# Kernel tuning notes

Measured on AMD Instinct MI355X. Metric: run time of the kernel, lower is better.

Reference implementation:

```python
import jax, jax.numpy as jnp
import numpy as np
import math

DIM = 768
HIDDEN = 3072
HEADS = 8
DEPTH = DIM // HEADS
EPS = 1e-5


def gelu_tanh(x):
    c = math.sqrt(2.0 / math.pi)
    return x * 0.5 * (1.0 + jnp.tanh(c * (x + 0.044715 * jnp.power(x, 3))))


def layer_norm(x, g, b):
    mu = jnp.mean(x, axis=-1, keepdims=True)
    var = jnp.mean(jnp.square(x - mu), axis=-1, keepdims=True)
    return (x - mu) * jax.lax.rsqrt(var + EPS) * g + b


def setup_inputs() -> dict:
    key = jax.random.key(0)
    ks = jax.random.split(key, 12)
    B, F, N = 2, 64, 128
    s = 0.02
    return {
        "q": jax.random.normal(ks[0], (B, F, N, DIM), jnp.float32),
        "k": jax.random.normal(ks[1], (B, F, N, DIM), jnp.float32),
        "v": jax.random.normal(ks[2], (B, F, N, DIM), jnp.float32),
        "ln1_g": jnp.ones((DIM,), jnp.float32),
        "ln1_b": jnp.zeros((DIM,), jnp.float32),
        "wq": jax.random.normal(ks[3], (DIM, DIM), jnp.float32) * s,
        "wk": jax.random.normal(ks[4], (DIM, DIM), jnp.float32) * s,
        "wv": jax.random.normal(ks[5], (DIM, DIM), jnp.float32) * s,
        "wo": jax.random.normal(ks[6], (DIM, DIM), jnp.float32) * s,
        "wo_b": jnp.zeros((DIM,), jnp.float32),
        "ln2_g": jnp.ones((DIM,), jnp.float32),
        "ln2_b": jnp.zeros((DIM,), jnp.float32),
        "w1": jax.random.normal(ks[7], (DIM, HIDDEN), jnp.float32) * s,
        "b1": jnp.zeros((HIDDEN,), jnp.float32),
        "w2": jax.random.normal(ks[8], (HIDDEN, DIM), jnp.float32) * s,
        "b2": jnpp if False else jnp.zeros((DIM,), jnp.float32),
    }


def reference(q, k, v, ln1_g, ln1_b, wq, wk, wv, wo, wo_b, ln2_g, ln2_b, w1, b1, w2, b2):
    # Shared norm1 applied to q, k, v (same params, as in the original)
    qn = layer_norm(q, ln1_g, ln1_b)
    kn = layer_norm(k, ln1_g, ln1_b)
    vn = layer_norm(v, ln1_g, ln1_b)

    B, F, N, _ = qn.shape
    # Projections (no bias on wq/wk/wv since att_bias=False)
    def split_heads(x):
        return x.reshape(B, F, N, HEADS, DEPTH).transpose(0, 1, 3, 2, 4)  # b f h n d

    qh = split_heads(qn @ wq)
    kh = split_heads(kn @ wk)
    vh = split_heads(vn @ wv)

    scale = DEPTH ** (-0.5)
    dots = jnp.einsum('bfhid,bfhjd->bfhij', qh, kh) * scale
    att_weight = jax.nn.softmax(dots, axis=-1)
    out = jnp.einsum('bfhij,bfhjd->bfhid', att_weight, vh)
    out = out.transpose(0, 1, 3, 2, 4).reshape(B, F, N, DIM)
    y = out @ wo + wo_b

    y = y + qn  # residual with normed q
    h = gelu_tanh(layer_norm(y, ln2_g, ln2_b) @ w1 + b1)
    out2 = h @ w2 + b2
    return out2 + y, att_weight
```

## Files before the change

kernel.cpp:

```cpp
#include <hip/hip_runtime.h>


#define NROWS 16384
#define TDIM 768
#define THID 3072
#define EPS 1e-5f

typedef short bf16x8 __attribute__((ext_vector_type(8)));
typedef float f32x4 __attribute__((ext_vector_type(4)));

__device__ __forceinline__ float b2f(unsigned short u) {
    union { unsigned int i; float f; } v; v.i = ((unsigned int)u) << 16; return v.f;
}
__device__ __forceinline__ unsigned short f2b(float f) {
    union { float f; unsigned int i; } v; v.f = f;
    unsigned int r = v.i + 0x7fffu + ((v.i >> 16) & 1u);
    return (unsigned short)(r >> 16);
}

__device__ __forceinline__ void async_copy16(const unsigned short* g, unsigned short* l) {
    __builtin_amdgcn_global_load_lds(
        (const __attribute__((address_space(1))) unsigned int*)g,
        (__attribute__((address_space(3))) unsigned int*)l,
        16, 0, 0);
}

__global__ __launch_bounds__(256) void cvt_t_kernel(
    const float* __restrict__ src, unsigned short* __restrict__ dst, int K, int N)
{
    __shared__ unsigned short tile[32][33];
    int n0 = blockIdx.x * 32, k0 = blockIdx.y * 32;
    int tx = threadIdx.x & 31, ty = threadIdx.x >> 5;
#pragma unroll
    for (int r = ty; r < 32; r += 8)
        tile[r][tx] = f2b(src[(size_t)(k0 + r) * N + n0 + tx]);
    __syncthreads();
#pragma unroll
    for (int r = ty; r < 32; r += 8)
        dst[(size_t)(n0 + r) * K + k0 + tx] = tile[tx][r];
}

template<bool IN_F32>
__global__ __launch_bounds__(256) void ln_kernel(
    const void* __restrict__ x0, const void* __restrict__ x1,
    const void* __restrict__ x2,
    const float* __restrict__ g, const float* __restrict__ bb,
    unsigned short* __restrict__ o0, unsigned short* __restrict__ o1,
    unsigned short* __restrict__ o2)
{
    int t = blockIdx.y;
    const void* x = (t == 0) ? x0 : (t == 1) ? x1 : x2;
    unsigned short* o = (t == 0) ? o0 : (t == 1) ? o1 : o2;
    size_t base = (size_t)blockIdx.x * TDIM;
    int tid = threadIdx.x;
    float v[3]; float sum = 0.f, sq = 0.f;
#pragma unroll
    for (int i = 0; i < 3; i++) {
        if constexpr (IN_F32) v[i] = ((const float*)x)[base + tid + i * 256];
        else v[i] = b2f(((const unsigned short*)x)[base + tid + i * 256]);
        sum += v[i]; sq += v[i] * v[i];
    }
#pragma unroll
    for (int o_ = 32; o_ > 0; o_ >>= 1) {
        sum += __shfl_down(sum, o_); sq += __shfl_down(sq, o_);
    }
    __shared__ float s1[4], s2[4];
    __shared__ float smu, srs;
    int wave = tid >> 6, lane = tid & 63;
    if (lane == 0) { s1[wave] = sum; s2[wave] = sq; }
    __syncthreads();
    if (tid == 0) {
        float S = s1[0] + s1[1] + s1[2] + s1[3];
        float Q = s2[0] + s2[1] + s2[2] + s2[3];
        float mu = S / (float)TDIM;
        float var = Q / (float)TDIM - mu * mu;
        smu = mu; srs = rsqrtf(var + EPS);
    }
    __syncthreads();
    float mu = smu, rs = srs;
#pragma unroll
    for (int i = 0; i < 3; i++) {
        int c = tid + i * 256;
        o[base + c] = f2b((v[i] - mu) * rs * g[c] + bb[c]);
    }
}

template<bool BIAS, bool RES, bool GELU, bool OUTF32>
__global__ __launch_bounds__(256) void gemm_kernel(
    const unsigned short* __restrict__ A, const unsigned short* __restrict__ BT,
    const float* __restrict__ bias, const unsigned short* __restrict__ resid,
    void* __restrict__ Cv, int M, int N, int K,
    size_t aStride, size_t bStride, size_t cStride)
{
    __shared__ unsigned short sA[128][32];
    __shared__ unsigned short sB[128][32];
    int tid = threadIdx.x;

    int nbx = gridDim.x;
    int nwg = nbx * gridDim.y;
    int bid = blockIdx.y * nbx + blockIdx.x;
    int xcd = bid & 7, loc = bid >> 3;
    int qc = nwg >> 3, rc = nwg & 7;
    int swz = (xcd < rc ? xcd * (qc + 1) : rc * (qc + 1) + (xcd - rc) * qc) + loc;
    int row0 = (swz / nbx) * 128;
    int col0 = (swz % nbx) * 128;

    int z = blockIdx.z;
    A  += (size_t)z * aStride;
    BT += (size_t)z * bStride;
    size_t zoff = (size_t)z * cStride;

    int wave = tid >> 6, lane = tid & 63;
    int wm = (wave >> 1) * 64, wn = (wave & 1) * 64;
    int cl = lane & 15, quad = lane >> 4;

    f32x4 acc[4][4];
#pragma unroll
    for (int i = 0; i < 4; i++)
#pragma unroll
        for (int j = 0; j < 4; j++) acc[i][j] = (f32x4){0.f, 0.f, 0.f, 0.f};

    const unsigned short* Arow = A + (size_t)row0 * K;
    const unsigned short* Brow = BT + (size_t)col0 * K;

    int c0 = wave * 128 + lane, c1 = c0 + 64;
    const unsigned short* aS0 = Arow + (size_t)(c0 >> 2) * K + ((c0 & 3) << 3);
    const unsigned short* aS1 = Arow + (size_t)(c1 >> 2) * K + ((c1 & 3) << 3);
    const unsigned short* bS0 = Brow + (size_t)(c0 >> 2) * K + ((c0 & 3) << 3);
    const unsigned short* bS1 = Brow + (size_t)(c1 >> 2) * K + ((c1 & 3) << 3);
    unsigned short* aD0 = &sA[0][0] + (size_t)(wave * 128) * 8;
    unsigned short* aD1 = aD0 + 64 * 8;
    unsigned short* bD0 = &sB[0][0] + (size_t)(wave * 128) * 8;
    unsigned short* bD1 = bD0 + 64 * 8;

    for (int k0 = 0; k0 < K; k0 += 32) {
        async_copy16(aS0 + k0, aD0);
        async_copy16(aS1 + k0, aD1);
        async_copy16(bS0 + k0, bD0);
        async_copy16(bS1 + k0, bD1);
        __syncthreads();
        bf16x8 af[4], bfr[4];
#pragma unroll
        for (int mi = 0; mi < 4; mi++)
            af[mi] = *(const bf16x8*)(&sA[wm + mi * 16 + cl][quad * 8]);
#pragma unroll
        for (int ni = 0; ni < 4; ni++)
            bfr[ni] = *(const bf16x8*)(&sB[wn + ni * 16 + cl][quad * 8]);
#pragma unroll
        for (int mi = 0; mi < 4; mi++)
#pragma unroll
            for (int ni = 0; ni < 4; ni++)
                acc[mi][ni] = __builtin_amdgcn_mfma_f32_16x16x32_bf16(
                    af[mi], bfr[ni], acc[mi][ni], 0, 0, 0);
        __syncthreads();
    }

    float bvv[4];
#pragma unroll
    for (int ni = 0; ni < 4; ni++) {
        if constexpr (BIAS) bvv[ni] = bias[col0 + wn + ni * 16 + cl];
        else bvv[ni] = 0.f;
    }
#pragma unroll
    for (int mi = 0; mi < 4; mi++) {
#pragma unroll
        for (int r = 0; r < 4; r++) {
            int gr = row0 + wm + mi * 16 + quad * 4 + r;
            size_t rb = (size_t)gr * N + col0 + wn + cl;
#pragma unroll
            for (int ni = 0; ni < 4; ni++) {
                float v = acc[mi][ni][r];
                if constexpr (BIAS) v += bvv[ni];
                if constexpr (GELU) {
                    float x = v;
                    float t = x + 0.044715f * x * x * x;
                    float e = __expf(-1.5957691216057308f * t);
                    v = x * __builtin_amdgcn_rcpf(1.0f + e);
                }
                if constexpr (RES) v += b2f(resid[rb + ni * 16]);
                size_t idx = rb + ni * 16 + zoff;
                if constexpr (OUTF32) ((float*)Cv)[idx] = v;
                else ((unsigned short*)Cv)[idx] = f2b(v);
            }
        }
    }
}

template<bool BIAS, bool GELU>
__global__ __launch_bounds__(512) void gemm256_kernel(
    const unsigned short* __restrict__ A, const unsigned short* __restrict__ BT,
    const float* __restrict__ bias, unsigned short* __restrict__ C,
    int N, int K)
{
    __shared__ unsigned short sA[2][256][32];
    __shared__ unsigned short sB[2][256][32];
    int tid = threadIdx.x;

    int nbx = gridDim.x;
    int nwg = nbx * gridDim.y;
    int bid = blockIdx.y * nbx + blockIdx.x;
    int xcd = bid & 7, loc = bid >> 3;
    int qc = nwg >> 3, rc = nwg & 7;
    int swz = (xcd < rc ? xcd * (qc + 1) : rc * (qc + 1) + (xcd - rc) * qc) + loc;
    int row0 = (swz / nbx) * 256;
    int col0 = (swz % nbx) * 256;

    int wave = tid >> 6, lane = tid & 63;
    int wr = wave >> 2, wc = wave & 3;
    int cl = lane & 15, quad = lane >> 4;
    int sl8 = (quad ^ ((cl >> 1) & 3)) << 3;

    size_t rowoff = (size_t)(tid >> 2) * K + (size_t)(((tid & 3) ^ ((tid >> 3) & 3)) << 3);
    const unsigned short* aS0 = A + (size_t)row0 * K + rowoff;
    const unsigned short* aS1 = aS0 + (size_t)128 * K;
    const unsigned short* bS0 = BT + (size_t)col0 * K + rowoff;
    const unsigned short* bS1 = bS0 + (size_t)128 * K;
    unsigned short* aD = &sA[0][0][0] + (wave * 64) * 8;
    unsigned short* bD = &sB[0][0][0] + (wave * 64) * 8;

    f32x4 acc[8][4];
#pragma unroll
    for (int i = 0; i < 8; i++)
#pragma unroll
        for (int j = 0; j < 4; j++) acc[i][j] = (f32x4){0.f, 0.f, 0.f, 0.f};

    int NT = K >> 5;
    async_copy16(aS0, aD);
    async_copy16(aS1, aD + 4096);
    async_copy16(bS0, bD);
    async_copy16(bS1, bD + 4096);

    for (int t = 0; t < NT; ++t) {
        int cur = t & 1;
        if (t + 1 < NT) {
            int nb = (cur ^ 1) * 8192;
            int ko = (t + 1) << 5;
            async_copy16(aS0 + ko, aD + nb);
            async_copy16(aS1 + ko, aD + nb + 4096);
            async_copy16(bS0 + ko, bD + nb);
            async_copy16(bS1 + ko, bD + nb + 4096);
            asm volatile("s_waitcnt vmcnt(4)" ::: "memory");
        } else {
            asm volatile("s_waitcnt vmcnt(0)" ::: "memory");
        }
        __builtin_amdgcn_s_barrier();
        __builtin_amdgcn_sched_barrier(0);
        const unsigned short* pA = &sA[cur][0][0];
        const unsigned short* pB = &sB[cur][0][0];
        bf16x8 bfr[4], af[4];
#pragma unroll
        for (int ni = 0; ni < 4; ni++)
            bfr[ni] = *(const bf16x8*)(pB + (wc * 64 + ni * 16 + cl) * 32 + sl8);
#pragma unroll
        for (int mi = 0; mi < 4; mi++)
            af[mi] = *(const bf16x8*)(pA + (wr * 128 + mi * 16 + cl) * 32 + sl8);
#pragma unroll
        for (int mi = 0; mi < 4; mi++)
#pragma unroll
            for (int ni = 0; ni < 4; ni++)
                acc[mi][ni] = __builtin_amdgcn_mfma_f32_16x16x32_bf16(
                    af[mi], bfr[ni], acc[mi][ni], 0, 0, 0);
#pragma unroll
        for (int mi = 0; mi < 4; mi++)
            af[mi] = *(const bf16x8*)(pA + (wr * 128 + 64 + mi * 16 + cl) * 32 + sl8);
#pragma unroll
        for (int mi = 0; mi < 4; mi++)
#pragma unroll
            for (int ni = 0; ni < 4; ni++)
                acc[mi + 4][ni] = __builtin_amdgcn_mfma_f32_16x16x32_bf16(
                    af[mi], bfr[ni], acc[mi + 4][ni], 0, 0, 0);
        __builtin_amdgcn_sched_barrier(0);
        __builtin_amdgcn_s_barrier();
        __builtin_amdgcn_sched_barrier(0);
    }

    float bvv[4];
#pragma unroll
    for (int ni = 0; ni < 4; ni++) {
        if constexpr (BIAS) bvv[ni] = bias[col0 + wc * 64 + ni * 16 + cl];
        else bvv[ni] = 0.f;
    }
#pragma unroll
    for (int mi = 0; mi < 8; mi++) {
#pragma unroll
        for (int r = 0; r < 4; r++) {
            int gr = row0 + wr * 128 + mi * 16 + quad * 4 + r;
            size_t rb = (size_t)gr * N + col0 + wc * 64 + cl;
#pragma unroll
            for (int ni = 0; ni < 4; ni++) {
                float v = acc[mi][ni][r] + bvv[ni];
                if constexpr (GELU) {
                    float x = v;
                    float tt = x + 0.044715f * x * x * x;
                    float e = __expf(-1.5957691216057308f * tt);
                    v = x * __builtin_amdgcn_rcpf(1.0f + e);
                }
                C[rb + ni * 16] = f2b(v);
            }
        }
    }
}

__global__ __launch_bounds__(256) void attn_fused_kernel(
    const unsigned short* __restrict__ qh, const unsigned short* __restrict__ kh,
    const unsigned short* __restrict__ vh, float* __restrict__ att,
    unsigned short* __restrict__ attout)
{
    __shared__ __align__(16) unsigned short smem[30464];
    __shared__ float wmax[2][128];
    __shared__ float wsum[2][128];
    __shared__ float sInv[128];
    unsigned short* sQ = smem;
    unsigned short* sK = smem + 12288;
    unsigned short* sP = smem;
    unsigned short* sVt = smem + 17408;

    int hb = blockIdx.x, g = hb >> 3, h = hb & 7;
    int tid = threadIdx.x;
    int wave = tid >> 6, lane = tid & 63;
    int cl = lane & 15, quad = lane >> 4;
    int wm = (wave >> 1) * 64, wn = (wave & 1) * 64;

    size_t rbase = (size_t)g * 128 * TDIM + (size_t)h * 96;

#pragma unroll
    for (int it = 0; it < 6; it++) {
        int cb = wave * 384 + it * 64;
        int c = cb + lane;
        int r = c / 12, dc = (c % 12) * 8;
        async_copy16(qh + rbase + (size_t)r * TDIM + dc, sQ + (size_t)cb * 8);
        async_copy16(kh + rbase + (size_t)r * TDIM + dc, sK + (size_t)cb * 8);
    }
    __syncthreads();

    f32x4 acc[4][4];
#pragma unroll
    for (int i = 0; i < 4; i++)
#pragma unroll
        for (int j = 0; j < 4; j++) acc[i][j] = (f32x4){0.f, 0.f, 0.f, 0.f};
#pragma unroll
    for (int kk = 0; kk < 3; kk++) {
        bf16x8 af[4], bfr[4];
#pragma unroll
        for (int mi = 0; mi < 4; mi++)
            af[mi] = *(const bf16x8*)(sQ + (size_t)(wm + mi * 16 + cl) * 96 + kk * 32 + quad * 8);
#pragma unroll
        for (int ni = 0; ni < 4; ni++)
            bfr[ni] = *(const bf16x8*)(sK + (size_t)(wn + ni * 16 + cl) * 96 + kk * 32 + quad * 8);
#pragma unroll
        for (int mi = 0; mi < 4; mi++)
#pragma unroll
            for (int ni = 0; ni < 4; ni++)
                acc[mi][ni] = __builtin_amdgcn_mfma_f32_16x16x32_bf16(
                    af[mi], bfr[ni], acc[mi][ni], 0, 0, 0);
    }

    const float scale = 0.10206207261596575f;
#pragma unroll
    for (int mi = 0; mi < 4; mi++)
#pragma unroll
        for (int ni = 0; ni < 4; ni++)
#pragma unroll
            for (int r = 0; r < 4; r++) acc[mi][ni][r] *= scale;
#pragma unroll
    for (int mi = 0; mi < 4; mi++) {
#pragma unroll
        for (int r = 0; r < 4; r++) {
            float m = fmaxf(fmaxf(acc[mi][0][r], acc[mi][1][r]),
                            fmaxf(acc[mi][2][r], acc[mi][3][r]));
            m = fmaxf(m, __shfl_xor(m, 1));
            m = fmaxf(m, __shfl_xor(m, 2));
            m = fmaxf(m, __shfl_xor(m, 4));
            m = fmaxf(m, __shfl_xor(m, 8));
            if (cl == 0) wmax[wn >> 6][wm + mi * 16 + quad * 4 + r] = m;
        }
    }
    __syncthreads();

    for (int c = tid; c < 1536; c += 256) {
        int kk2 = c / 12, dc2 = (c % 12) * 8;
        uint4 t_ = *(const uint4*)(vh + rbase + (size_t)kk2 * TDIM + dc2);
        unsigned short* tp = (unsigned short*)&t_;
#pragma unroll
        for (int j = 0; j < 8; j++) {
            int jj = (j + tid) & 7;
            sVt[(size_t)(dc2 + jj) * 136 + kk2] = tp[jj];
        }
    }

#pragma unroll
    for (int mi = 0; mi < 4; mi++) {
#pragma unroll
        for (int r = 0; r < 4; r++) {
            int row = wm + mi * 16 + quad * 4 + r;
            float rm = fmaxf(wmax[0][row], wmax[1][row]);
            float s = 0.f;
#pragma unroll
            for (int ni = 0; ni < 4; ni++) {
                float e = __expf(acc[mi][ni][r] - rm);
                acc[mi][ni][r] = e;
                s += e;
            }
            s += __shfl_xor(s, 1);
            s += __shfl_xor(s, 2);
            s += __shfl_xor(s, 4);
            s += __shfl_xor(s, 8);
            if (cl == 0) wsum[wn >> 6][row] = s;
#pragma unroll
            for (int ni = 0; ni < 4; ni++)
                sP[(size_t)row * 136 + wn + ni * 16 + cl] = f2b(acc[mi][ni][r]);
        }
    }
    __syncthreads();

    if (tid < 128) sInv[tid] = 1.0f / (wsum[0][tid] + wsum[1][tid]);
    __syncthreads();

    size_t pbase = (size_t)hb * 128 * 128;
#pragma unroll
    for (int mi = 0; mi < 4; mi++) {
#pragma unroll
        for (int r = 0; r < 4; r++) {
            int row = wm + mi * 16 + quad * 4 + r;
            float iv = sInv[row];
#pragma unroll
            for (int ni = 0; ni < 4; ni++)
                att[pbase + (size_t)row * 128 + wn + ni * 16 + cl] =
                    acc[mi][ni][r] * iv;
        }
    }

    int wm2 = wave * 32;
    f32x4 acc2[2][6];
#pragma unroll
    for (int i = 0; i < 2; i++)
#pragma unroll
        for (int j = 0; j < 6; j++) acc2[i][j] = (f32x4){0.f, 0.f, 0.f, 0.f};
#pragma unroll
    for (int ks = 0; ks < 4; ks++) {
        bf16x8 pa[2], vb[6];
#pragma unroll
        for (int mi2 = 0; mi2 < 2; mi2++)
            pa[mi2] = *(const bf16x8*)(sP + (size_t)(wm2 + mi2 * 16 + cl) * 136 + ks * 32 + quad * 8);
#pragma unroll
        for (int ni2 = 0; ni2 < 6; ni2++)
            vb[ni2] = *(const bf16x8*)(sVt + (size_t)(ni2 * 16 + cl) * 136 + ks * 32 + quad * 8);
#pragma unroll
        for (int mi2 = 0; mi2 < 2; mi2++)
#pragma unroll
            for (int ni2 = 0; ni2 < 6; ni2++)
                acc2[mi2][ni2] = __builtin_amdgcn_mfma_f32_16x16x32_bf16(
                    pa[mi2], vb[ni2], acc2[mi2][ni2], 0, 0, 0);
    }
#pragma unroll
    for (int mi2 = 0; mi2 < 2; mi2++) {
#pragma unroll
        for (int r = 0; r < 4; r++) {
            int row = wm2 + mi2 * 16 + quad * 4 + r;
            float iv = sInv[row];
#pragma unroll
            for (int ni2 = 0; ni2 < 6; ni2++) {
                int d = ni2 * 16 + cl;
                attout[rbase + (size_t)row * TDIM + d] =
                    f2b(acc2[mi2][ni2][r] * iv);
            }
        }
    }
}

extern "C" void kernel_launch(void* const* d_in, const int* in_sizes, int n_in,
                              void* d_out, int out_size, void* d_ws, size_t ws_size,
                              hipStream_t stream)
{
    const float* q     = (const float*)d_in[0];
    const float* k     = (const float*)d_in[1];
    const float* v     = (const float*)d_in[2];
    const float* ln1_g = (const float*)d_in[3];
    const float* ln1_b = (const float*)d_in[4];
    const float* wq    = (const float*)d_in[5];
    const float* wk    = (const float*)d_in[6];
    const float* wv    = (const float*)d_in[7];
    const float* wo    = (const float*)d_in[8];
    const float* wo_b  = (const float*)d_in[9];
    const float* ln2_g = (const float*)d_in[10];
    const float* ln2_b = (const float*)d_in[11];
    const float* w1    = (const float*)d_in[12];
    const float* b1    = (const float*)d_in[13];
    const float* w2    = (const float*)d_in[14];
    const float* b2    = (const float*)d_in[15];

    float* out0 = (float*)d_out;
    const size_t S = (size_t)NROWS * TDIM;
    float* att = out0 + S;
    unsigned short* ws = (unsigned short*)d_ws;
    if (ws_size < 7 * S * sizeof(unsigned short)) return;

    const size_t W = (size_t)TDIM * TDIM;
    const size_t W2 = (size_t)TDIM * THID;

    unsigned short* qn     = ws;
    unsigned short* kn     = ws + S;
    unsigned short* vn     = ws + 2 * S;
    unsigned short* qh     = ws + 3 * S;
    unsigned short* wqkvoT = ws + 6 * S;
    unsigned short* attout = ws + S;
    unsigned short* y      = ws + 2 * S;
    unsigned short* ln2y   = ws;
    unsigned short* w1T    = ws + S;
    unsigned short* w2T    = ws + S + W2;
    unsigned short* hbuf   = ws + 3 * S;

    dim3 blk(256);
    cvt_t_kernel<<<dim3(24, 24), blk, 0, stream>>>(wq, wqkvoT + 0 * W, TDIM, TDIM);
    cvt_t_kernel<<<dim3(24, 24), blk, 0, stream>>>(wk, wqkvoT + 1 * W, TDIM, TDIM);
    cvt_t_kernel<<<dim3(24, 24), blk, 0, stream>>>(wv, wqkvoT + 2 * W, TDIM, TDIM);
    cvt_t_kernel<<<dim3(24, 24), blk, 0, stream>>>(wo, wqkvoT + 3 * W, TDIM, TDIM);
    ln_kernel<true><<<dim3(NROWS, 3), blk, 0, stream>>>(
        q, k, v, ln1_g, ln1_b, qn, kn, vn);
    gemm_kernel<false, false, false, false><<<dim3(6, 128, 3), blk, 0, stream>>>(
        qn, wqkvoT, nullptr, nullptr, qh, NROWS, TDIM, TDIM, S, W, S);
    attn_fused_kernel<<<dim3(1024), blk, 0, stream>>>(qh, qh + S, qh + 2 * S, att, attout);
    gemm_kernel<true, true, false, false><<<dim3(6, 128), blk, 0, stream>>>(
        attout, wqkvoT + 3 * W, wo_b, qn, y, NROWS, TDIM, TDIM, 0, 0, 0);
    cvt_t_kernel<<<dim3(96, 24), blk, 0, stream>>>(w1, w1T, TDIM, THID);
    cvt_t_kernel<<<dim3(24, 96), blk, 0, stream>>>(w2, w2T, THID, TDIM);
    ln_kernel<false><<<dim3(NROWS, 1), blk, 0, stream>>>(
        y, y, y, ln2_g, ln2_b, ln2y, ln2y, ln2y);
    gemm256_kernel<true, true><<<dim3(12, 64), dim3(512), 0, stream>>>(
        ln2y, w1T, b1, hbuf, THID, TDIM);
    gemm_kernel<true, true, false, true><<<dim3(6, 128), blk, 0, stream>>>(
        hbuf, w2T, b2, y, out0, NROWS, TDIM, THID, 0, 0, 0);
}
```

Measured before the change: 691.4 us.

## Deepen gemm256 pipeline to four LDS stages with prefetch distance two

Replaces the double-buffered LDS tiles in the 256x256 GEMM with a four-slot ring and issues global-to-LDS copies two K-steps ahead. The loads are split into halves interleaved with the two MFMA phases, with barriers and s_setprio raising priority around MFMA blocks. The aim is to hide global memory latency behind compute, at the cost of doubling LDS use (128KB), which lowers occupancy and adds barriers per iteration.

```diff
diff --git a/kernel.cpp b/kernel.cpp
--- a/kernel.cpp
+++ b/kernel.cpp
@@ -192,8 +192,7 @@
     const float* __restrict__ bias, unsigned short* __restrict__ C,
     int N, int K)
 {
-    __shared__ unsigned short sA[2][256][32];
-    __shared__ unsigned short sB[2][256][32];
+    __shared__ unsigned short lds[4][2][8192];
     int tid = threadIdx.x;
 
     int nbx = gridDim.x;
@@ -215,8 +214,8 @@
     const unsigned short* aS1 = aS0 + (size_t)128 * K;
     const unsigned short* bS0 = BT + (size_t)col0 * K + rowoff;
     const unsigned short* bS1 = bS0 + (size_t)128 * K;
-    unsigned short* aD = &sA[0][0][0] + (wave * 64) * 8;
-    unsigned short* bD = &sB[0][0][0] + (wave * 64) * 8;
+    int d0 = wave * 64 * 8;
+    int d1 = (512 + wave * 64) * 8;
 
     f32x4 acc[8][4];
 #pragma unroll
@@ -225,53 +224,70 @@
         for (int j = 0; j < 4; j++) acc[i][j] = (f32x4){0.f, 0.f, 0.f, 0.f};
 
     int NT = K >> 5;
-    async_copy16(aS0, aD);
-    async_copy16(aS1, aD + 4096);
-    async_copy16(bS0, bD);
-    async_copy16(bS1, bD + 4096);
-
-    for (int t = 0; t < NT; ++t) {
-        int cur = t & 1;
-        if (t + 1 < NT) {
-            int nb = (cur ^ 1) * 8192;
-            int ko = (t + 1) << 5;
-            async_copy16(aS0 + ko, aD + nb);
-            async_copy16(aS1 + ko, aD + nb + 4096);
-            async_copy16(bS0 + ko, bD + nb);
-            async_copy16(bS1 + ko, bD + nb + 4096);
+    async_copy16(aS0, &lds[0][0][d0]);
+    async_copy16(bS0, &lds[0][1][d0]);
+    async_copy16(aS1, &lds[0][0][d1]);
+    async_copy16(bS1, &lds[0][1][d1]);
+    async_copy16(aS0 + 32, &lds[1][0][d0]);
+    async_copy16(bS0 + 32, &lds[1][1][d0]);
+    async_copy16(aS1 + 32, &lds[1][0][d1]);
+    async_copy16(bS1 + 32, &lds[1][1][d1]);
+    asm volatile("s_waitcnt vmcnt(4)" ::: "memory");
+    __builtin_amdgcn_s_barrier();
+
+    for (int T = 0; T < NT; ++T) {
+        const unsigned short* pA = &lds[T & 3][0][0];
+        const unsigned short* pB = &lds[T & 3][1][0];
+        bool pre = (T + 2) < NT;
+        int sp = (T + 2) & 3;
+        int ko = (T + 2) << 5;
+        bf16x8 bfr[4], af[4];
+#pragma unroll
+        for (int ni = 0; ni < 4; ni++)
+            bfr[ni] = *(const bf16x8*)(pB + (wc * 64 + ni * 16 + cl) * 32 + sl8);
+#pragma unroll
+        for (int mi = 0; mi < 4; mi++)
+            af[mi] = *(const bf16x8*)(pA + (wr * 128 + mi * 16 + cl) * 32 + sl8);
+        if (pre) {
+            async_copy16(aS0 + ko, &lds[sp][0][d0]);
+            async_copy16(bS0 + ko, &lds[sp][1][d0]);
+        }
+        __builtin_amdgcn_s_barrier();
+        asm volatile("s_waitcnt lgkmcnt(0)" ::: "memory");
+        __builtin_amdgcn_sched_barrier(0);
+        __builtin_amdgcn_s_setprio(1);
+#pragma unroll
+        for (int mi = 0; mi < 4; mi++)
+#pragma unroll
+            for (int ni = 0; ni < 4; ni++)
+                acc[mi][ni] = __builtin_amdgcn_mfma_f32_16x16x32_bf16(
+                    af[mi], bfr[ni], acc[mi][ni], 0, 0, 0);
+        __builtin_amdgcn_s_setprio(0);
+        __builtin_amdgcn_sched_barrier(0);
+        __builtin_amdgcn_s_barrier();
+#pragma unroll
+        for (int mi = 0; mi < 4; mi++)
+            af[mi] = *(const bf16x8*)(pA + (wr * 128 + 64 + mi * 16 + cl) * 32 + sl8);
+        if (pre) {
+            async_copy16(aS1 + ko, &lds[sp][0][d1]);
+            async_copy16(bS1 + ko, &lds[sp][1][d1]);
             asm volatile("s_waitcnt vmcnt(4)" ::: "memory");
         } else {
             asm volatile("s_waitcnt vmcnt(0)" ::: "memory");
         }
         __builtin_amdgcn_s_barrier();
+        asm volatile("s_waitcnt lgkmcnt(0)" ::: "memory");
         __builtin_amdgcn_sched_barrier(0);
-        const unsigned short* pA = &sA[cur][0][0];
-        const unsigned short* pB = &sB[cur][0][0];
-        bf16x8 bfr[4], af[4];
-#pragma unroll
-        for (int ni = 0; ni < 4; ni++)
-            bfr[ni] = *(const bf16x8*)(pB + (wc * 64 + ni * 16 + cl) * 32 + sl8);
-#pragma unroll
-        for (int mi = 0; mi < 4; mi++)
-            af[mi] = *(const bf16x8*)(pA + (wr * 128 + mi * 16 + cl) * 32 + sl8);
-#pragma unroll
-        for (int mi = 0; mi < 4; mi++)
-#pragma unroll
-            for (int ni = 0; ni < 4; ni++)
-                acc[mi][ni] = __builtin_amdgcn_mfma_f32_16x16x32_bf16(
-                    af[mi], bfr[ni], acc[mi][ni], 0, 0, 0);
-#pragma unroll
-        for (int mi = 0; mi < 4; mi++)
-            af[mi] = *(const bf16x8*)(pA + (wr * 128 + 64 + mi * 16 + cl) * 32 + sl8);
+        __builtin_amdgcn_s_setprio(1);
 #pragma unroll
         for (int mi = 0; mi < 4; mi++)
 #pragma unroll
             for (int ni = 0; ni < 4; ni++)
                 acc[mi + 4][ni] = __builtin_amdgcn_mfma_f32_16x16x32_bf16(
                     af[mi], bfr[ni], acc[mi + 4][ni], 0, 0, 0);
+        __builtin_amdgcn_s_setprio(0);
         __builtin_amdgcn_sched_barrier(0);
         __builtin_amdgcn_s_barrier();
-        __builtin_amdgcn_sched_barrier(0);
     }
 
     float bvv[4];
```

Result: no change. 678.4 us (-1.9%).
